# Performance work log

Measured on AMD Instinct MI355X. Metric: run time of the kernel, lower is better.

The kernel has to match this reference:

```python
import jax, jax.numpy as jnp
import numpy as np

N, K = 16384, 32          # num bboxes, context size
IN_F, HID = 608, 384      # in_features, hidden_dim
ALPHA = 0.2               # LeakyReLU slope
NEG_INF = -9e15


def setup_inputs() -> dict:
    key = jax.random.key(0)
    k1, k2, k3, k4, k5, k6, k7, k8 = jax.random.split(key, 8)
    h_i = jax.random.normal(k1, (N, IN_F), dtype=jnp.float32)
    idx = jax.random.randint(k2, (N, K), 0, N)
    pad = jax.random.uniform(k3, (N, K)) < 0.2
    context_indices = jnp.where(pad, -1, idx).astype(jnp.int64)
    s_in = 1.0 / np.sqrt(IN_F)
    s_a = 1.0 / np.sqrt(2 * HID)
    W_i = jax.random.uniform(k4, (IN_F, HID), minval=-s_in, maxval=s_in, dtype=jnp.float32)
    W_j = jax.random.uniform(k5, (IN_F, HID), minval=-s_in, maxval=s_in, dtype=jnp.float32)
    a_i = jax.random.uniform(k6, (HID,), minval=-s_a, maxval=s_a, dtype=jnp.float32)
    a_j = jax.random.uniform(k7, (HID,), minval=-s_a, maxval=s_a, dtype=jnp.float32)
    a_b = jax.random.uniform(k8, (1,), minval=-s_a, maxval=s_a, dtype=jnp.float32)
    return {"h_i": h_i, "context_indices": context_indices,
            "W_i": W_i, "W_j": W_j, "a_i": a_i, "a_j": a_j, "a_b": a_b}


def reference(h_i, context_indices, W_i, W_j, a_i, a_j, a_b):
    n = h_i.shape[0]
    Wh_i = h_i @ W_i                          # [N, H]
    # W_j has no bias, so projecting then gathering (zero pad row) equals
    # gathering zero-padded features then projecting.
    Wh_all = h_i @ W_j                        # [N, H]
    Wh_pad = jnp.concatenate([Wh_all, jnp.zeros((1, HID), Wh_all.dtype)], axis=0)
    idx = jnp.where(context_indices >= 0, context_indices, n)   # -1 -> zero row
    Wh_j = Wh_pad[idx]                        # [N, K, H] gather
    # attention_layer(concat(Wh_i, Wh_j)) == Wh_i@a_i + Wh_j@a_j + b
    scores = (Wh_i @ a_i)[:, None] + Wh_j @ a_j + a_b[0]        # [N, K]
    scores = jnp.where(scores > 0, scores, ALPHA * scores)      # LeakyReLU
    scores = jnp.where(context_indices >= 0, scores, NEG_INF)   # mask padding
    att = jax.nn.softmax(scores, axis=1)                        # [N, K]
    h_prime = jnp.einsum('nk,nkh->nh', att, Wh_j)               # [N, H]
    return h_prime
```

## Files before the change

kernel.cpp:

```cpp
#include <hip/hip_runtime.h>
#include <hip/hip_bf16.h>

typedef unsigned short u16;
typedef unsigned int u32;
typedef __attribute__((ext_vector_type(8))) __bf16 bf16x8;
typedef __attribute__((ext_vector_type(4))) float f32x4;

#define KCTX 32
#define INF_ 608
#define HID_ 384

#define WH_OFF 0
#define BT_OFF 12582912
#define V_OFF  13049856
#define SJ_OFF 13052288

__device__ __forceinline__ float bfu(u16 u)  { return __uint_as_float(((u32)u) << 16); }
__device__ __forceinline__ float bflo(u32 u) { return __uint_as_float(u << 16); }
__device__ __forceinline__ float bfhi(u32 u) { return __uint_as_float(u & 0xffff0000u); }
__device__ __forceinline__ u16 f2bf(float x) {
  u32 u = __float_as_uint(x);
  return (u16)((u + 0x7fffu + ((u >> 16) & 1u)) >> 16);
}
__device__ __forceinline__ void async_ld16(const void* g, void* l) {
  __builtin_amdgcn_global_load_lds(
      (const __attribute__((address_space(1))) u32*)g,
      (__attribute__((address_space(3))) u32*)l, 16, 0, 0);
}

__device__ __forceinline__ int detect_f32(const u32* hw) {
  const u32 w = hw[threadIdx.x & 63];
  const int e = (int)((w >> 7) & 0xffu);
  const unsigned long long mb = __ballot(e > 134 || e < 100);
  return __popcll(mb) >= 16;
}
__device__ __forceinline__ int detect_i64(const int* ci) {
  const int hi = ci[2 * (threadIdx.x & 63) + 1];
  const unsigned long long mz = __ballot(hi == 0 || hi == -1);
  return __popcll(mz) >= 48;
}

__global__ __launch_bounds__(256) void prep_kernel(
    const void* __restrict__ h, const void* __restrict__ Wi,
    const void* __restrict__ Wj, const void* __restrict__ ai,
    u16* __restrict__ Bt, float* __restrict__ v, float* __restrict__ sj) {
  __shared__ u16 tile[64][65];
  const int f32m = detect_f32((const u32*)h);
  const int bid = blockIdx.x, tid = threadIdx.x;
  if (bid < 60) {
    const int ft = bid / 6, ht = bid - ft * 6;
    const int f0 = ft * 64, h0 = ht * 64;
    const int ln = tid & 63, fg = tid >> 6;
#pragma unroll
    for (int rr = 0; rr < 16; ++rr) {
      const int fl = fg * 16 + rr;
      const int f = f0 + fl;
      if (f < INF_)
        tile[fl][ln] = f32m ? f2bf(((const float*)Wj)[(size_t)f * HID_ + h0 + ln])
                            : ((const u16*)Wj)[(size_t)f * HID_ + h0 + ln];
    }
    __syncthreads();
#pragma unroll
    for (int rr = 0; rr < 16; ++rr) {
      const int hl = fg * 16 + rr;
      const int f = f0 + ln;
      if (f < INF_) Bt[(size_t)(h0 + hl) * INF_ + f] = tile[ln][hl];
    }
  } else if (bid < 63) {
    const int t = (bid - 60) * 256 + tid;
    if (t < INF_) {
      float s = 0.f;
      if (f32m) {
        const float4* wi = (const float4*)((const float*)Wi + (size_t)t * HID_);
        const float4* a4 = (const float4*)ai;
        for (int c = 0; c < 96; ++c) {
          float4 x = wi[c], y = a4[c];
          s += x.x * y.x + x.y * y.y + x.z * y.z + x.w * y.w;
        }
      } else {
        const uint4* wi = (const uint4*)((const u16*)Wi + (size_t)t * HID_);
        const uint4* a4 = (const uint4*)ai;
        for (int c = 0; c < 48; ++c) {
          uint4 x = wi[c], y = a4[c];
          s += bflo(x.x) * bflo(y.x) + bfhi(x.x) * bfhi(y.x)
             + bflo(x.y) * bflo(y.y) + bfhi(x.y) * bfhi(y.y)
             + bflo(x.z) * bflo(y.z) + bfhi(x.z) * bfhi(y.z)
             + bflo(x.w) * bflo(y.w) + bfhi(x.w) * bfhi(y.w);
        }
      }
      v[t] = s;
    }
  } else {
#pragma unroll 8
    for (int j = 0; j < 64; ++j) sj[j * 256 + tid] = 0.f;
  }
}

__global__ __launch_bounds__(256, 2) void gemm_kernel(
    const void* __restrict__ A, const u16* __restrict__ Bt,
    u16* __restrict__ C, const void* __restrict__ aj, float* __restrict__ sj) {
  __shared__ __align__(16) u16 As[128][32];
  __shared__ __align__(16) u16 Bs[128][32];
  const int f32m = detect_f32((const u32*)A);
  const int tid  = threadIdx.x;
  const int lane = tid & 63;
  const int wave = tid >> 6;
  const int row0 = blockIdx.x * 128;
  const int col0 = blockIdx.y * 128;
  const int wm = (wave & 1) * 64;
  const int wn = (wave >> 1) * 64;

  f32x4 acc[4][4];
#pragma unroll
  for (int i = 0; i < 4; ++i)
#pragma unroll
    for (int j = 0; j < 4; ++j) acc[i][j] = (f32x4){0.f, 0.f, 0.f, 0.f};

  const int c0 = tid, c1 = tid + 256;
  const int rA0 = c0 >> 2, kc0 = (c0 & 3) * 16;
  const int rA1 = c1 >> 2, kc1 = (c1 & 3) * 16;
  const char* Ab  = (const char*)A;
  const char* Btb = (const char*)Bt;

  for (int kt = 0; kt < 19; ++kt) {
    const size_t kb = (size_t)kt * 64;
    if (!f32m) {
      async_ld16(Ab + (size_t)(row0 + rA0) * 1216 + kb + kc0, (char*)As + c0 * 16);
      async_ld16(Ab + (size_t)(row0 + rA1) * 1216 + kb + kc1, (char*)As + c1 * 16);
    } else {
      const float* Af = (const float*)A;
#pragma unroll
      for (int j = 0; j < 4; ++j) {
        const int c = tid + j * 256;
        const int r = c >> 3, q = c & 7;
        const float4 fv = *(const float4*)(Af + (size_t)(row0 + r) * INF_ + kt * 32 + q * 4);
        ushort4 sv;
        sv.x = f2bf(fv.x); sv.y = f2bf(fv.y); sv.z = f2bf(fv.z); sv.w = f2bf(fv.w);
        *(ushort4*)&As[r][q * 4] = sv;
      }
    }
    async_ld16(Btb + (size_t)(col0 + rA0) * 1216 + kb + kc0, (char*)Bs + c0 * 16);
    async_ld16(Btb + (size_t)(col0 + rA1) * 1216 + kb + kc1, (char*)Bs + c1 * 16);
    __syncthreads();

    const int kk = (lane >> 4) * 8;
    const int lm0 = lane & 15;
    bf16x8 af[4], bfr[4];
#pragma unroll
    for (int i = 0; i < 4; ++i) af[i]  = *(const bf16x8*)&As[wm + i * 16 + lm0][kk];
#pragma unroll
    for (int i = 0; i < 4; ++i) bfr[i] = *(const bf16x8*)&Bs[wn + i * 16 + lm0][kk];
#pragma unroll
    for (int im = 0; im < 4; ++im)
#pragma unroll
      for (int in = 0; in < 4; ++in)
        acc[im][in] = __builtin_amdgcn_mfma_f32_16x16x32_bf16(
            af[im], bfr[in], acc[im][in], 0, 0, 0);
    __syncthreads();
  }

  const int lm = lane & 15, lq = lane >> 4;
#pragma unroll
  for (int im = 0; im < 4; ++im)
#pragma unroll
    for (int in = 0; in < 4; ++in) {
      const int colg = col0 + wn + in * 16 + lm;
#pragma unroll
      for (int r = 0; r < 4; ++r) {
        const int rowg = row0 + wm + im * 16 + lq * 4 + r;
        C[(size_t)rowg * HID_ + colg] = f2bf(acc[im][in][r]);
      }
    }
  float ajv[4];
#pragma unroll
  for (int in = 0; in < 4; ++in) {
    const int colg = col0 + wn + in * 16 + lm;
    ajv[in] = f32m ? ((const float*)aj)[colg] : bfu(((const u16*)aj)[colg]);
  }
#pragma unroll
  for (int im = 0; im < 4; ++im)
#pragma unroll
    for (int r = 0; r < 4; ++r) {
      float p = acc[im][0][r] * ajv[0] + acc[im][1][r] * ajv[1]
              + acc[im][2][r] * ajv[2] + acc[im][3][r] * ajv[3];
      p += __shfl_xor(p, 1); p += __shfl_xor(p, 2);
      p += __shfl_xor(p, 4); p += __shfl_xor(p, 8);
      if (lm == 0) atomicAdd(&sj[row0 + wm + im * 16 + lq * 4 + r], p);
    }
}

__global__ __launch_bounds__(256) void attn_kernel(
    const void* __restrict__ h, const int* __restrict__ ci,
    const float* __restrict__ v, const float* __restrict__ sj,
    const void* __restrict__ ab, const u16* __restrict__ Wh,
    void* __restrict__ out) {
  __shared__ float att_s[4][32];
  __shared__ int   idx_s[4][32];
  const int f32m = detect_f32((const u32*)h);
  const int i64  = detect_i64(ci);
  const int wv = threadIdx.x >> 6;
  const int lane = threadIdx.x & 63;
  const int n = blockIdx.x * 4 + wv;

  float sum = 0.f;
  if (f32m) {
    const float4* hrow = (const float4*)((const float*)h + (size_t)n * INF_);
    const float4* v4 = (const float4*)v;
    for (int c = lane; c < 152; c += 64) {
      float4 u = hrow[c], w = v4[c];
      sum += u.x * w.x + u.y * w.y + u.z * w.z + u.w * w.w;
    }
  } else {
    const uint4* hrow = (const uint4*)((const u16*)h + (size_t)n * INF_);
    const float4* v4 = (const float4*)v;
    for (int c = lane; c < 76; c += 64) {
      uint4 u = hrow[c];
      float4 w0 = v4[2 * c], w1 = v4[2 * c + 1];
      sum += bflo(u.x) * w0.x + bfhi(u.x) * w0.y + bflo(u.y) * w0.z + bfhi(u.y) * w0.w
           + bflo(u.z) * w1.x + bfhi(u.z) * w1.y + bflo(u.w) * w1.z + bfhi(u.w) * w1.w;
    }
  }
#pragma unroll
  for (int o = 32; o; o >>= 1) sum += __shfl_xor(sum, o);

  if (lane < 32) {
    const size_t t = (size_t)n * KCTX + lane;
    int idx;
    if (i64) { int lo = ci[2 * t], hi = ci[2 * t + 1]; idx = (hi < 0) ? -1 : lo; }
    else     { idx = ci[t]; }
    const bool valid = idx >= 0;
    const float sjv = valid ? sj[idx] : 0.f;
    const float bias = f32m ? ((const float*)ab)[0] : bfu(((const u16*)ab)[0]);
    float raw = sum + sjv + bias;
    float lr = raw > 0.f ? raw : 0.2f * raw;
    float s = valid ? lr : -9e15f;
    float m = s;
#pragma unroll
    for (int o = 16; o; o >>= 1) m = fmaxf(m, __shfl_xor(m, o, 32));
    float p = __expf(s - m);
    float d = p;
#pragma unroll
    for (int o = 16; o; o >>= 1) d += __shfl_xor(d, o, 32);
    att_s[wv][lane] = valid ? p / d : 0.f;
    idx_s[wv][lane] = valid ? idx : 0;
  }
  __syncthreads();

  if (lane < 48) {
    float a0 = 0, a1 = 0, a2 = 0, a3 = 0, a4 = 0, a5 = 0, a6 = 0, a7 = 0;
#pragma unroll 4
    for (int k = 0; k < KCTX; ++k) {
      const float w = att_s[wv][k];
      const uint4* row = (const uint4*)(Wh + (u32)idx_s[wv][k] * HID_);
      const uint4 q = row[lane];
      a0 += w * bflo(q.x); a1 += w * bfhi(q.x);
      a2 += w * bflo(q.y); a3 += w * bfhi(q.y);
      a4 += w * bflo(q.z); a5 += w * bfhi(q.z);
      a6 += w * bflo(q.w); a7 += w * bfhi(q.w);
    }
    if (f32m) {
      float4* o4 = (float4*)out + (size_t)n * 96 + lane * 2;
      o4[0] = (float4){a0, a1, a2, a3};
      o4[1] = (float4){a4, a5, a6, a7};
    } else {
      uint4 o;
      o.x = (u32)f2bf(a0) | ((u32)f2bf(a1) << 16);
      o.y = (u32)f2bf(a2) | ((u32)f2bf(a3) << 16);
      o.z = (u32)f2bf(a4) | ((u32)f2bf(a5) << 16);
      o.w = (u32)f2bf(a6) | ((u32)f2bf(a7) << 16);
      ((uint4*)out)[(size_t)n * 48 + lane] = o;
    }
  }
}

extern "C" void kernel_launch(void* const* d_in, const int* in_sizes, int n_in,
                              void* d_out, int out_size, void* d_ws, size_t ws_size,
                              hipStream_t stream) {
  const void* h  = d_in[0];
  const int*  ci = (const int*)d_in[1];
  const void* Wi = d_in[2];
  const void* Wj = d_in[3];
  const void* aj = d_in[5];
  const void* ai = d_in[4];
  const void* ab = d_in[6];

  char* ws = (char*)d_ws;
  u16*   Wh = (u16*)(ws + WH_OFF);
  u16*   Bt = (u16*)(ws + BT_OFF);
  float* v  = (float*)(ws + V_OFF);
  float* sj = (float*)(ws + SJ_OFF);

  prep_kernel<<<64, 256, 0, stream>>>(h, Wi, Wj, ai, Bt, v, sj);
  dim3 g(128, 3);
  gemm_kernel<<<g, 256, 0, stream>>>(h, Bt, Wh, aj, sj);
  attn_kernel<<<4096, 256, 0, stream>>>(h, ci, v, sj, ab, Wh, d_out);
}
```

Baseline: 176.9 us.

## Pre-convert h to bf16 in a separate pass and fuse the s_i dot product

A new conv kernel reads fp32 h once, writes a bf16 copy and computes the per-row h·v score. The GEMM can then use async LDS loads for A instead of converting fp32 in the inner loop, and the attention kernel no longer re-reads h to compute s_i. The v reduction in prep is parallelized across 16 lanes per row. The attention gather drops shared memory and the barrier in favour of shuffles, and skips rows whose weight is zero. The cost is one extra launch plus writing and re-reading the bf16 copy of h.

```diff
diff --git a/kernel.cpp b/kernel.cpp
--- a/kernel.cpp
+++ b/kernel.cpp
@@ -10,10 +10,14 @@
 #define INF_ 608
 #define HID_ 384
 
-#define WH_OFF 0
-#define BT_OFF 12582912
-#define V_OFF  13049856
-#define SJ_OFF 13052288
+#define HB_OFF  0
+#define WH_OFF  19922944
+#define BT_OFF  32505856
+#define V_OFF   32972800
+#define SI_OFF  32975232
+#define SJ_OFF  33040768
+#define AJF_OFF 33106304
+#define ABF_OFF 33107840
 
 __device__ __forceinline__ float bfu(u16 u)  { return __uint_as_float(((u32)u) << 16); }
 __device__ __forceinline__ float bflo(u32 u) { return __uint_as_float(u << 16); }
@@ -43,7 +47,9 @@
 __global__ __launch_bounds__(256) void prep_kernel(
     const void* __restrict__ h, const void* __restrict__ Wi,
     const void* __restrict__ Wj, const void* __restrict__ ai,
-    u16* __restrict__ Bt, float* __restrict__ v, float* __restrict__ sj) {
+    const void* __restrict__ aj, const void* __restrict__ ab,
+    u16* __restrict__ Bt, float* __restrict__ v, float* __restrict__ sj,
+    float* __restrict__ ajf, float* __restrict__ abf) {
   __shared__ u16 tile[64][65];
   const int f32m = detect_f32((const u32*)h);
   const int bid = blockIdx.x, tid = threadIdx.x;
@@ -66,21 +72,22 @@
       const int f = f0 + ln;
       if (f < INF_) Bt[(size_t)(h0 + hl) * INF_ + f] = tile[ln][hl];
     }
-  } else if (bid < 63) {
-    const int t = (bid - 60) * 256 + tid;
+  } else if (bid < 98) {
+    const int t = (bid - 60) * 16 + (tid >> 4);
+    const int sl = tid & 15;
     if (t < INF_) {
       float s = 0.f;
       if (f32m) {
         const float4* wi = (const float4*)((const float*)Wi + (size_t)t * HID_);
         const float4* a4 = (const float4*)ai;
-        for (int c = 0; c < 96; ++c) {
+        for (int c = sl; c < 96; c += 16) {
           float4 x = wi[c], y = a4[c];
           s += x.x * y.x + x.y * y.y + x.z * y.z + x.w * y.w;
         }
       } else {
         const uint4* wi = (const uint4*)((const u16*)Wi + (size_t)t * HID_);
         const uint4* a4 = (const uint4*)ai;
-        for (int c = 0; c < 48; ++c) {
+        for (int c = sl; c < 48; c += 16) {
           uint4 x = wi[c], y = a4[c];
           s += bflo(x.x) * bflo(y.x) + bfhi(x.x) * bfhi(y.x)
              + bflo(x.y) * bflo(y.y) + bfhi(x.y) * bfhi(y.y)
@@ -88,20 +95,63 @@
              + bflo(x.w) * bflo(y.w) + bfhi(x.w) * bfhi(y.w);
         }
       }
-      v[t] = s;
+      s += __shfl_xor(s, 1); s += __shfl_xor(s, 2);
+      s += __shfl_xor(s, 4); s += __shfl_xor(s, 8);
+      if (sl == 0) v[t] = s;
     }
   } else {
 #pragma unroll 8
     for (int j = 0; j < 64; ++j) sj[j * 256 + tid] = 0.f;
-  }
+    for (int j = tid; j < HID_; j += 256)
+      ajf[j] = f32m ? ((const float*)aj)[j] : bfu(((const u16*)aj)[j]);
+    if (tid == 0)
+      abf[0] = f32m ? ((const float*)ab)[0] : bfu(((const u16*)ab)[0]);
+  }
+}
+
+__global__ __launch_bounds__(256) void conv_kernel(
+    const void* __restrict__ h, const float* __restrict__ v,
+    u16* __restrict__ hb, float* __restrict__ si) {
+  const int f32m = detect_f32((const u32*)h);
+  const int wv = threadIdx.x >> 6, lane = threadIdx.x & 63;
+  const int n = blockIdx.x * 4 + wv;
+  uint4* hbrow = (uint4*)(hb + (size_t)n * INF_);
+  const float4* v4 = (const float4*)v;
+  float sum = 0.f;
+  if (f32m) {
+    const float4* hr = (const float4*)((const float*)h + (size_t)n * INF_);
+    for (int c = lane; c < 76; c += 64) {
+      float4 x0 = hr[2 * c], x1 = hr[2 * c + 1];
+      uint4 o;
+      o.x = (u32)f2bf(x0.x) | ((u32)f2bf(x0.y) << 16);
+      o.y = (u32)f2bf(x0.z) | ((u32)f2bf(x0.w) << 16);
+      o.z = (u32)f2bf(x1.x) | ((u32)f2bf(x1.y) << 16);
+      o.w = (u32)f2bf(x1.z) | ((u32)f2bf(x1.w) << 16);
+      hbrow[c] = o;
+      float4 w0 = v4[2 * c], w1 = v4[2 * c + 1];
+      sum += x0.x * w0.x + x0.y * w0.y + x0.z * w0.z + x0.w * w0.w
+           + x1.x * w1.x + x1.y * w1.y + x1.z * w1.z + x1.w * w1.w;
+    }
+  } else {
+    const uint4* hr = (const uint4*)((const u16*)h + (size_t)n * INF_);
+    for (int c = lane; c < 76; c += 64) {
+      uint4 x = hr[c];
+      hbrow[c] = x;
+      float4 w0 = v4[2 * c], w1 = v4[2 * c + 1];
+      sum += bflo(x.x) * w0.x + bfhi(x.x) * w0.y + bflo(x.y) * w0.z + bfhi(x.y) * w0.w
+           + bflo(x.z) * w1.x + bfhi(x.z) * w1.y + bflo(x.w) * w1.z + bfhi(x.w) * w1.w;
+    }
+  }
+#pragma unroll
+  for (int o = 32; o; o >>= 1) sum += __shfl_xor(sum, o);
+  if (lane == 0) si[n] = sum;
 }
 
 __global__ __launch_bounds__(256, 2) void gemm_kernel(
-    const void* __restrict__ A, const u16* __restrict__ Bt,
-    u16* __restrict__ C, const void* __restrict__ aj, float* __restrict__ sj) {
+    const u16* __restrict__ A, const u16* __restrict__ Bt,
+    u16* __restrict__ C, const float* __restrict__ ajf, float* __restrict__ sj) {
   __shared__ __align__(16) u16 As[128][32];
   __shared__ __align__(16) u16 Bs[128][32];
-  const int f32m = detect_f32((const u32*)A);
   const int tid  = threadIdx.x;
   const int lane = tid & 63;
   const int wave = tid >> 6;
@@ -124,21 +174,8 @@
 
   for (int kt = 0; kt < 19; ++kt) {
     const size_t kb = (size_t)kt * 64;
-    if (!f32m) {
-      async_ld16(Ab + (size_t)(row0 + rA0) * 1216 + kb + kc0, (char*)As + c0 * 16);
-      async_ld16(Ab + (size_t)(row0 + rA1) * 1216 + kb + kc1, (char*)As + c1 * 16);
-    } else {
-      const float* Af = (const float*)A;
-#pragma unroll
-      for (int j = 0; j < 4; ++j) {
-        const int c = tid + j * 256;
-        const int r = c >> 3, q = c & 7;
-        const float4 fv = *(const float4*)(Af + (size_t)(row0 + r) * INF_ + kt * 32 + q * 4);
-        ushort4 sv;
-        sv.x = f2bf(fv.x); sv.y = f2bf(fv.y); sv.z = f2bf(fv.z); sv.w = f2bf(fv.w);
-        *(ushort4*)&As[r][q * 4] = sv;
-      }
-    }
+    async_ld16(Ab  + (size_t)(row0 + rA0) * 1216 + kb + kc0, (char*)As + c0 * 16);
+    async_ld16(Ab  + (size_t)(row0 + rA1) * 1216 + kb + kc1, (char*)As + c1 * 16);
     async_ld16(Btb + (size_t)(col0 + rA0) * 1216 + kb + kc0, (char*)Bs + c0 * 16);
     async_ld16(Btb + (size_t)(col0 + rA1) * 1216 + kb + kc1, (char*)Bs + c1 * 16);
     __syncthreads();
@@ -173,10 +210,7 @@
     }
   float ajv[4];
 #pragma unroll
-  for (int in = 0; in < 4; ++in) {
-    const int colg = col0 + wn + in * 16 + lm;
-    ajv[in] = f32m ? ((const float*)aj)[colg] : bfu(((const u16*)aj)[colg]);
-  }
+  for (int in = 0; in < 4; ++in) ajv[in] = ajf[col0 + wn + in * 16 + lm];
 #pragma unroll
   for (int im = 0; im < 4; ++im)
 #pragma unroll
@@ -191,38 +225,15 @@
 
 __global__ __launch_bounds__(256) void attn_kernel(
     const void* __restrict__ h, const int* __restrict__ ci,
-    const float* __restrict__ v, const float* __restrict__ sj,
-    const void* __restrict__ ab, const u16* __restrict__ Wh,
+    const float* __restrict__ si, const float* __restrict__ sj,
+    const float* __restrict__ abf, const u16* __restrict__ Wh,
     void* __restrict__ out) {
-  __shared__ float att_s[4][32];
-  __shared__ int   idx_s[4][32];
   const int f32m = detect_f32((const u32*)h);
   const int i64  = detect_i64(ci);
-  const int wv = threadIdx.x >> 6;
-  const int lane = threadIdx.x & 63;
+  const int wv = threadIdx.x >> 6, lane = threadIdx.x & 63;
   const int n = blockIdx.x * 4 + wv;
 
-  float sum = 0.f;
-  if (f32m) {
-    const float4* hrow = (const float4*)((const float*)h + (size_t)n * INF_);
-    const float4* v4 = (const float4*)v;
-    for (int c = lane; c < 152; c += 64) {
-      float4 u = hrow[c], w = v4[c];
-      sum += u.x * w.x + u.y * w.y + u.z * w.z + u.w * w.w;
-    }
-  } else {
-    const uint4* hrow = (const uint4*)((const u16*)h + (size_t)n * INF_);
-    const float4* v4 = (const float4*)v;
-    for (int c = lane; c < 76; c += 64) {
-      uint4 u = hrow[c];
-      float4 w0 = v4[2 * c], w1 = v4[2 * c + 1];
-      sum += bflo(u.x) * w0.x + bfhi(u.x) * w0.y + bflo(u.y) * w0.z + bfhi(u.y) * w0.w
-           + bflo(u.z) * w1.x + bfhi(u.z) * w1.y + bflo(u.w) * w1.z + bfhi(u.w) * w1.w;
-    }
-  }
-#pragma unroll
-  for (int o = 32; o; o >>= 1) sum += __shfl_xor(sum, o);
-
+  float att = 0.f; int idxv = 0;
   if (lane < 32) {
     const size_t t = (size_t)n * KCTX + lane;
     int idx;
@@ -230,8 +241,7 @@
     else     { idx = ci[t]; }
     const bool valid = idx >= 0;
     const float sjv = valid ? sj[idx] : 0.f;
-    const float bias = f32m ? ((const float*)ab)[0] : bfu(((const u16*)ab)[0]);
-    float raw = sum + sjv + bias;
+    float raw = si[n] + sjv + abf[0];
     float lr = raw > 0.f ? raw : 0.2f * raw;
     float s = valid ? lr : -9e15f;
     float m = s;
@@ -241,23 +251,24 @@
     float d = p;
 #pragma unroll
     for (int o = 16; o; o >>= 1) d += __shfl_xor(d, o, 32);
-    att_s[wv][lane] = valid ? p / d : 0.f;
-    idx_s[wv][lane] = valid ? idx : 0;
-  }
-  __syncthreads();
-
-  if (lane < 48) {
-    float a0 = 0, a1 = 0, a2 = 0, a3 = 0, a4 = 0, a5 = 0, a6 = 0, a7 = 0;
+    att = valid ? p / d : 0.f;
+    idxv = valid ? idx : 0;
+  }
+
+  float a0 = 0, a1 = 0, a2 = 0, a3 = 0, a4 = 0, a5 = 0, a6 = 0, a7 = 0;
 #pragma unroll 4
-    for (int k = 0; k < KCTX; ++k) {
-      const float w = att_s[wv][k];
-      const uint4* row = (const uint4*)(Wh + (u32)idx_s[wv][k] * HID_);
-      const uint4 q = row[lane];
+  for (int k = 0; k < KCTX; ++k) {
+    const float w = __shfl(att, k);
+    const int   j = __shfl(idxv, k);
+    if (w != 0.f && lane < 48) {
+      const uint4 q = ((const uint4*)(Wh + (u32)j * HID_))[lane];
       a0 += w * bflo(q.x); a1 += w * bfhi(q.x);
       a2 += w * bflo(q.y); a3 += w * bfhi(q.y);
       a4 += w * bflo(q.z); a5 += w * bfhi(q.z);
       a6 += w * bflo(q.w); a7 += w * bfhi(q.w);
     }
+  }
+  if (lane < 48) {
     if (f32m) {
       float4* o4 = (float4*)out + (size_t)n * 96 + lane * 2;
       o4[0] = (float4){a0, a1, a2, a3};
@@ -280,18 +291,23 @@
   const int*  ci = (const int*)d_in[1];
   const void* Wi = d_in[2];
   const void* Wj = d_in[3];
+  const void* ai = d_in[4];
   const void* aj = d_in[5];
-  const void* ai = d_in[4];
   const void* ab = d_in[6];
 
   char* ws = (char*)d_ws;
-  u16*   Wh = (u16*)(ws + WH_OFF);
-  u16*   Bt = (u16*)(ws + BT_OFF);
-  float* v  = (float*)(ws + V_OFF);
-  float* sj = (float*)(ws + SJ_OFF);
-
-  prep_kernel<<<64, 256, 0, stream>>>(h, Wi, Wj, ai, Bt, v, sj);
+  u16*   hb  = (u16*)(ws + HB_OFF);
+  u16*   Wh  = (u16*)(ws + WH_OFF);
+  u16*   Bt  = (u16*)(ws + BT_OFF);
+  float* v   = (float*)(ws + V_OFF);
+  float* si  = (float*)(ws + SI_OFF);
+  float* sj  = (float*)(ws + SJ_OFF);
+  float* ajf = (float*)(ws + AJF_OFF);
+  float* abf = (float*)(ws + ABF_OFF);
+
+  prep_kernel<<<99, 256, 0, stream>>>(h, Wi, Wj, ai, aj, ab, Bt, v, sj, ajf, abf);
+  conv_kernel<<<4096, 256, 0, stream>>>(h, v, hb, si);
   dim3 g(128, 3);
-  gemm_kernel<<<g, 256, 0, stream>>>(h, Bt, Wh, aj, sj);
-  attn_kernel<<<4096, 256, 0, stream>>>(h, ci, v, sj, ab, Wh, d_out);
-}
+  gemm_kernel<<<g, 256, 0, stream>>>(hb, Bt, Wh, ajf, sj);
+  attn_kernel<<<4096, 256, 0, stream>>>(h, ci, si, sj, abf, Wh, d_out);
+}
```

New measurement: 166.0 us. 1.07x faster.
